# Optimization experiments

Hardware: AMD Instinct MI355X
Metric: run time of the kernel (lower is better)

## Reference

```python
import jax, jax.numpy as jnp
import numpy as np

N = 50000      # nodes
E = 800000     # edges (avg degree 16)
G = 8          # graphs in batch
D = 128        # in/hidden feats
C = 10         # classes


def setup_inputs() -> dict:
    key = jax.random.key(0)
    ks = jax.random.split(key, 9)
    x = jax.random.normal(ks[0], (N, D), dtype=jnp.float32)
    edge_index = jax.random.randint(ks[1], (2, E), 0, N)
    node2graph = jnp.sort(jax.random.randint(ks[2], (N,), 0, G))
    s = 1.0 / np.sqrt(D)
    W1 = jax.random.normal(ks[3], (D, D), dtype=jnp.float32) * s
    b1 = jnp.zeros((D,), jnp.float32)
    W2 = jax.random.normal(ks[4], (D, D), dtype=jnp.float32) * s
    b2 = jnp.zeros((D,), jnp.float32)
    Wl = jax.random.normal(ks[5], (D, C), dtype=jnp.float32) * s
    bl = jnp.zeros((C,), jnp.float32)
    return {"x": x, "edge_index": edge_index, "node2graph": node2graph,
            "W1": W1, "b1": b1, "W2": W2, "b2": b2, "Wl": Wl, "bl": bl}


def _graph_conv(h, src, dst, out_isqrt, in_isqrt, W, b):
    # DGL GraphConv, norm='both': D_in^{-1/2} A D_out^{-1/2} (h W) + b
    h = (h * out_isqrt[:, None]) @ W
    agg = jax.ops.segment_sum(h[src], dst, num_segments=N)  # SpMM gather/scatter
    return agg * in_isqrt[:, None] + b


def reference(x, edge_index, node2graph, W1, b1, W2, b2, Wl, bl):
    src, dst = edge_index[0], edge_index[1]
    ones_e = jnp.ones((E,), jnp.float32)
    out_deg = jnp.clip(jax.ops.segment_sum(ones_e, src, num_segments=N), 1.0)
    in_deg = jnp.clip(jax.ops.segment_sum(ones_e, dst, num_segments=N), 1.0)
    out_isqrt = jax.lax.rsqrt(out_deg)
    in_isqrt = jax.lax.rsqrt(in_deg)

    h = jax.nn.relu(_graph_conv(x, src, dst, out_isqrt, in_isqrt, W1, b1))
    h = jax.nn.relu(_graph_conv(h, src, dst, out_isqrt, in_isqrt, W2, b2))

    # AvgPooling: per-graph mean of node features
    sums = jax.ops.segment_sum(h, node2graph, num_segments=G)
    counts = jnp.clip(jax.ops.segment_sum(jnp.ones((N,), jnp.float32), node2graph, num_segments=G), 1.0)
    hg = sums / counts[:, None]

    logits = hg @ Wl + bl
    return jax.nn.softmax(logits, axis=1)
```

## Files before the change

kernel.cpp:

```cpp
#include <hip/hip_runtime.h>
#include <stdint.h>

#define FD 128
#define NG 8
#define NC 10
#define MAXB 1024
#define CHUNK 4096

typedef __attribute__((ext_vector_type(8))) short bf16x8;
typedef __attribute__((ext_vector_type(4))) float f32x4;
typedef __attribute__((ext_vector_type(2))) float f32x2;

__device__ __forceinline__ float bf2f(uint16_t u){
    union { uint32_t i; float f; } v; v.i = ((uint32_t)u) << 16; return v.f;
}
__device__ __forceinline__ uint16_t f2bf(float f){
    union { float f; uint32_t i; } v; v.f = f;
    uint32_t r = v.i + 0x7fff + ((v.i >> 16) & 1);
    return (uint16_t)(r >> 16);
}

#if __has_builtin(__builtin_amdgcn_cvt_pk_f32_fp8) && __has_builtin(__builtin_amdgcn_cvt_pk_fp8_f32)
__device__ __forceinline__ f32x2 fp8lo2f(uint32_t p){
    return __builtin_amdgcn_cvt_pk_f32_fp8((int)p, false);
}
__device__ __forceinline__ f32x2 fp8hi2f(uint32_t p){
    return __builtin_amdgcn_cvt_pk_f32_fp8((int)p, true);
}
__device__ __forceinline__ uint32_t pk4fp8(float a, float b, float c, float d){
    int u = 0;
    u = __builtin_amdgcn_cvt_pk_fp8_f32(a, b, u, false);
    u = __builtin_amdgcn_cvt_pk_fp8_f32(c, d, u, true);
    return (uint32_t)u;
}
#else
__device__ __forceinline__ float fp8tof(uint32_t b){
    union { uint32_t i; float f; } v;
    v.i = ((b & 0x7f) << 20) | ((b & 0x80) << 24);
    return v.f * 0x1p120f;
}
__device__ __forceinline__ f32x2 fp8lo2f(uint32_t p){
    return (f32x2){fp8tof(p & 0xff), fp8tof((p >> 8) & 0xff)};
}
__device__ __forceinline__ f32x2 fp8hi2f(uint32_t p){
    return (f32x2){fp8tof((p >> 16) & 0xff), fp8tof((p >> 24) & 0xff)};
}
__device__ __forceinline__ uint32_t f2fp8(float f){
    union { float f; uint32_t i; } v; v.f = f;
    uint32_t s = (v.i >> 24) & 0x80;
    float a = fabsf(f);
    if (a < 0x1p-10f) return s;
    if (a > 448.f) return s | 0x7e;
    v.f = a;
    uint32_t r = v.i + 0x7ffff + ((v.i >> 20) & 1);
    int e = (int)(r >> 23) - 127 + 7;
    uint32_t m = (r >> 20) & 7;
    if (e <= 0){
        uint32_t q = (uint32_t)(a * 512.f + 0.5f);
        return s | (q > 7 ? 8 : q);
    }
    if (e > 15) return s | 0x7e;
    return s | ((uint32_t)e << 3) | m;
}
__device__ __forceinline__ uint32_t pk4fp8(float a, float b, float c, float d){
    return (uint32_t)f2fp8(a) | ((uint32_t)f2fp8(b)<<8) |
           ((uint32_t)f2fp8(c)<<16) | ((uint32_t)f2fp8(d)<<24);
}
#endif

__global__ __launch_bounds__(256) void k_prep(const float* __restrict__ W1,
        const float* __restrict__ W2, uint16_t* Wf1, uint16_t* Wf2,
        const int* __restrict__ ei, int E, int B, int C, int shift,
        int* __restrict__ cnt, float* __restrict__ pool,
        unsigned long long* __restrict__ state, int* __restrict__ counters){
    int t = threadIdx.x;
    if (blockIdx.x < 128){
        int id = blockIdx.x*256 + t;
        int w = id >> 14;
        int r = id & 16383;
        int j = r & 7, frag = r >> 3;
        int lane = frag & 63, t2 = frag >> 6;
        int n = t2 & 7, kk = t2 >> 3;
        int k = kk*32 + (lane>>4)*8 + j;
        int col = n*16 + (lane&15);
        float v = (w ? W2 : W1)[k*128 + col];
        (w ? Wf2 : Wf1)[r] = f2bf(v);
        if (blockIdx.x == 0){
            for (int i = t; i < NG*FD; i += 256) pool[i] = 0.f;
            for (int i = t; i < 1024; i += 256) state[i] = 0ull;
            if (t < 8) counters[t] = 0;
        }
        return;
    }
    __shared__ int hd[MAXB], hs[MAXB];
    int c = blockIdx.x - 128;
    for (int i=t;i<B;i+=256){ hd[i]=0; hs[i]=0; }
    __syncthreads();
    int e0 = c*CHUNK, e1 = min(E, e0+CHUNK);
    for (int e = e0+t; e < e1; e += 256){
        int s = ei[e], d = ei[E+e];
        atomicAdd(&hd[d>>shift], 1);
        atomicAdd(&hs[s>>shift], 1);
    }
    __syncthreads();
    for (int i=t;i<B;i+=256){
        cnt[(size_t)i*C + c]     = hd[i];
        cnt[(size_t)(B+i)*C + c] = hs[i];
    }
}

#define SEPT 16
#define STILE 4096
__global__ __launch_bounds__(256) void k_scan(int* __restrict__ a, int M,
        unsigned long long* __restrict__ state, int* __restrict__ ticket){
    __shared__ int bid_s, exc_s;
    __shared__ int s[256];
    int t = threadIdx.x;
    if (t == 0) bid_s = atomicAdd(ticket, 1);
    __syncthreads();
    int bid = bid_s;
    int base = bid*STILE + t*SEPT;
    int v[SEPT]; int sum = 0;
    #pragma unroll
    for (int i=0;i<SEPT;i++){ int idx=base+i; int x=(idx<M)?a[idx]:0; v[i]=sum; sum+=x; }
    s[t]=sum; __syncthreads();
    for (int o=1;o<256;o<<=1){ int x=(t>=o)?s[t-o]:0; __syncthreads(); s[t]+=x; __syncthreads(); }
    int tot = s[255];
    int te = s[t]-sum;
    if (t == 0){
        unsigned long long pub = ((bid==0) ? (2ull<<62) : (1ull<<62)) | (unsigned long long)(unsigned)tot;
        __hip_atomic_store(&state[bid], pub, __ATOMIC_RELEASE, __HIP_MEMORY_SCOPE_AGENT);
        int exc = 0;
        if (bid > 0){
            int p = bid-1;
            while (true){
                unsigned long long st = __hip_atomic_load(&state[p], __ATOMIC_ACQUIRE, __HIP_MEMORY_SCOPE_AGENT);
                unsigned long long fl = st >> 62;
                if (fl == 2ull){ exc += (int)(unsigned)st; break; }
                if (fl == 1ull){ exc += (int)(unsigned)st; p--; }
            }
            __hip_atomic_store(&state[bid],
                (2ull<<62) | (unsigned long long)(unsigned)(exc + tot),
                __ATOMIC_RELEASE, __HIP_MEMORY_SCOPE_AGENT);
        }
        exc_s = exc;
    }
    __syncthreads();
    int exc = exc_s;
    #pragma unroll
    for (int i=0;i<SEPT;i++){ int idx=base+i; if (idx<M) a[idx]=exc+te+v[i]; }
}

__global__ __launch_bounds__(256) void k_scatter(const int* __restrict__ ei, int E,
        int B, int C, int shift, const int* __restrict__ scan,
        uint32_t* __restrict__ tempD, uint16_t* __restrict__ tempS){
    __shared__ int cd[MAXB], cs[MAXB];
    int t = threadIdx.x, c = blockIdx.x;
    for (int i=t;i<B;i+=256){
        cd[i] = scan[(size_t)i*C + c];
        cs[i] = scan[(size_t)(B+i)*C + c] - E;
    }
    __syncthreads();
    int e0 = c*CHUNK, e1 = min(E, e0+CHUNK);
    int lmask = (1<<shift) - 1;
    for (int e = e0+t; e < e1; e += 256){
        int s = ei[e], d = ei[E+e];
        int p = atomicAdd(&cd[d>>shift], 1);
        tempD[p] = ((uint32_t)(d & lmask) << 20) | (uint32_t)s;
        int q = atomicAdd(&cs[s>>shift], 1);
        tempS[q] = (uint16_t)s;
    }
}

__global__ __launch_bounds__(256) void k_build2(const uint32_t* __restrict__ tempD,
        const uint16_t* __restrict__ tempS, const int* __restrict__ scan,
        int B, int C, int shift, int E, int N,
        int* __restrict__ row_off, int* __restrict__ csr, int* __restrict__ deg_out){
    __shared__ int cnt[MAXB];
    __shared__ int offl[MAXB];
    int b = blockIdx.x, t = threadIdx.x;
    int range = 1<<shift, nb0 = b<<shift;
    int seg0 = scan[(size_t)b*C];
    int seg1 = (b+1<B) ? scan[(size_t)(b+1)*C] : E;
    for (int i=t;i<range;i+=256) cnt[i]=0;
    __syncthreads();
    for (int i=seg0+t; i<seg1; i+=256)
        atomicAdd(&cnt[tempD[i]>>20], 1);
    __syncthreads();
    if (t==0){ int run=0; for (int i=0;i<range;i++){ offl[i]=run; run+=cnt[i]; } }
    __syncthreads();
    for (int i=t;i<range;i+=256){
        int node = nb0+i;
        if (node < N) row_off[node] = seg0 + offl[i];
    }
    if (b==B-1 && t==0) row_off[N] = E;
    for (int i=t;i<range;i+=256) cnt[i] = offl[i];
    __syncthreads();
    for (int i=seg0+t; i<seg1; i+=256){
        uint32_t v = tempD[i];
        int p = atomicAdd(&cnt[v>>20], 1);
        csr[seg0 + p] = (int)(v & 0xFFFFFu);
    }
    __syncthreads();
    int sg0 = scan[(size_t)(B+b)*C] - E;
    int sg1 = ((b+1<B) ? scan[(size_t)(B+b+1)*C] : 2*E) - E;
    for (int i=t;i<range;i+=256) cnt[i]=0;
    __syncthreads();
    for (int i=sg0+t; i<sg1; i+=256)
        atomicAdd(&cnt[(int)tempS[i] - nb0], 1);
    __syncthreads();
    for (int i=t;i<range;i+=256){
        int node = nb0+i;
        if (node < N) deg_out[node] = cnt[i];
    }
}

__global__ __launch_bounds__(256) void k_gemm(const void* __restrict__ A,
        const uint16_t* __restrict__ Wf, const int* __restrict__ deg_out,
        uint8_t* __restrict__ out8, int nrows, int amode){
    int t = threadIdx.x;
    int wave = t>>6, lane = t&63, quad = lane>>4, low = lane&15;

    int rowA  = blockIdx.x*64 + wave*16 + low;
    int rowAc = min(rowA, nrows-1);

    bf16x8 ah[4];
    if (amode){
        const uint16_t* arow = (const uint16_t*)A + (size_t)rowAc*FD;
        #pragma unroll
        for (int kk=0;kk<4;kk++)
            ah[kk] = *(const bf16x8*)(arow + kk*32 + quad*8);
    } else {
        const float* arow = (const float*)A + (size_t)rowAc*FD;
        #pragma unroll
        for (int kk=0;kk<4;kk++){
            f32x4 f0 = *(const f32x4*)(arow + kk*32 + quad*8);
            f32x4 f1 = *(const f32x4*)(arow + kk*32 + quad*8 + 4);
            #pragma unroll
            for (int j=0;j<4;j++) ah[kk][j]   = (short)f2bf(f0[j]);
            #pragma unroll
            for (int j=0;j<4;j++) ah[kk][j+4] = (short)f2bf(f1[j]);
        }
    }

    f32x4 acc[8];
    #pragma unroll
    for (int n=0;n<8;n++) acc[n] = (f32x4){0.f,0.f,0.f,0.f};

    #pragma unroll
    for (int kk=0;kk<4;kk++){
        #pragma unroll
        for (int n=0;n<8;n++){
            bf16x8 bh = *(const bf16x8*)(Wf + ((size_t)((kk*8+n)*64 + lane))*8);
            acc[n] = __builtin_amdgcn_mfma_f32_16x16x32_bf16(bh, ah[kk], acc[n], 0, 0, 0);
        }
    }

    if (rowA < nrows){
        float sc = rsqrtf((float)max(deg_out[rowA], 1));
        uint8_t* orow = out8 + (size_t)rowA*FD;
        #pragma unroll
        for (int n=0;n<8;n++){
            uint32_t pk = pk4fp8(acc[n][0]*sc, acc[n][1]*sc, acc[n][2]*sc, acc[n][3]*sc);
            *(uint32_t*)(orow + n*16 + quad*4) = pk;
        }
    }
}

__device__ __forceinline__ void spmm_row(const uint2* __restrict__ tp,
        const int* __restrict__ csr_src, int e0, int e1, int l, int qb,
        f32x2& a01, f32x2& a23, f32x2& a45, f32x2& a67){
    for (int base = e0; base < e1; base += 16){
        int my = 0;
        if (base + l < e1) my = csr_src[base + l];
        int cnt = min(16, e1 - base);
        for (int j0 = 0; j0 < cnt; j0 += 8){
            int ss[8];
            #pragma unroll
            for (int k=0;k<8;k++)
                ss[k] = __shfl(my, qb + min(j0 + k, cnt-1));
            uint2 p[8];
            #pragma unroll
            for (int k=0;k<8;k++)
                p[k] = tp[(size_t)ss[k]*16 + l];
            #pragma unroll
            for (int k=0;k<8;k++){
                if (j0 + k < cnt){
                    a01 += fp8lo2f(p[k].x); a23 += fp8hi2f(p[k].x);
                    a45 += fp8lo2f(p[k].y); a67 += fp8hi2f(p[k].y);
                }
            }
        }
    }
}

__global__ __launch_bounds__(256) void k_spmm_gemm(const uint8_t* __restrict__ tmp8,
        const int* __restrict__ row_off, const int* __restrict__ csr_src,
        const float* __restrict__ bias, const uint16_t* __restrict__ Wf,
        const int* __restrict__ deg_out, uint8_t* __restrict__ out8, int N){
    __shared__ __align__(16) uint16_t hsrow[64][136];
    int tid = threadIdx.x;
    int l = tid & 15, qid = tid >> 4, qb = (tid & 63) & 48;
    const uint2* tp = (const uint2*)tmp8;
    f32x4 bv0 = *(const f32x4*)(bias + l*8);
    f32x4 bv1 = *(const f32x4*)(bias + l*8 + 4);
    #pragma unroll
    for (int i = 0; i < 4; i++){
        int rowL = qid*4 + i;
        int node = blockIdx.x*64 + rowL;
        int e0 = 0, e1 = 0;
        if (node < N){ e0 = row_off[node]; e1 = row_off[node+1]; }
        f32x2 a01={0.f,0.f}, a23={0.f,0.f}, a45={0.f,0.f}, a67={0.f,0.f};
        spmm_row(tp, csr_src, e0, e1, l, qb, a01, a23, a45, a67);
        float isq = rsqrtf((float)max(e1 - e0, 1));
        float r0 = fmaxf(a01.x*isq + bv0[0], 0.f);
        float r1 = fmaxf(a01.y*isq + bv0[1], 0.f);
        float r2 = fmaxf(a23.x*isq + bv0[2], 0.f);
        float r3 = fmaxf(a23.y*isq + bv0[3], 0.f);
        float r4 = fmaxf(a45.x*isq + bv1[0], 0.f);
        float r5 = fmaxf(a45.y*isq + bv1[1], 0.f);
        float r6 = fmaxf(a67.x*isq + bv1[2], 0.f);
        float r7 = fmaxf(a67.y*isq + bv1[3], 0.f);
        uint4 o;
        o.x = (uint32_t)f2bf(r0) | ((uint32_t)f2bf(r1) << 16);
        o.y = (uint32_t)f2bf(r2) | ((uint32_t)f2bf(r3) << 16);
        o.z = (uint32_t)f2bf(r4) | ((uint32_t)f2bf(r5) << 16);
        o.w = (uint32_t)f2bf(r6) | ((uint32_t)f2bf(r7) << 16);
        if (node >= N) o = (uint4){0u,0u,0u,0u};
        *(uint4*)(&hsrow[rowL][l*8]) = o;
    }
    __syncthreads();
    int wave = tid>>6, lane = tid&63, quad = lane>>4, low = lane&15;
    int rowL = wave*16 + low;
    int rowA = blockIdx.x*64 + rowL;
    bf16x8 ah[4];
    #pragma unroll
    for (int kk=0;kk<4;kk++)
        ah[kk] = *(const bf16x8*)(&hsrow[rowL][kk*32 + quad*8]);
    f32x4 acc[8];
    #pragma unroll
    for (int n=0;n<8;n++) acc[n] = (f32x4){0.f,0.f,0.f,0.f};
    #pragma unroll
    for (int kk=0;kk<4;kk++){
        #pragma unroll
        for (int n=0;n<8;n++){
            bf16x8 bh = *(const bf16x8*)(Wf + ((size_t)((kk*8+n)*64 + lane))*8);
            acc[n] = __builtin_amdgcn_mfma_f32_16x16x32_bf16(bh, ah[kk], acc[n], 0, 0, 0);
        }
    }
    if (rowA < N){
        float sc = rsqrtf((float)max(deg_out[rowA], 1));
        uint8_t* orow = out8 + (size_t)rowA*FD;
        #pragma unroll
        for (int n=0;n<8;n++){
            uint32_t pk = pk4fp8(acc[n][0]*sc, acc[n][1]*sc, acc[n][2]*sc, acc[n][3]*sc);
            *(uint32_t*)(orow + n*16 + quad*4) = pk;
        }
    }
}

__global__ __launch_bounds__(256) void k_spmm_pool(const uint8_t* __restrict__ tmp8,
        const int* __restrict__ row_off, const int* __restrict__ csr_src,
        const float* __restrict__ bias, const int* __restrict__ n2g,
        float* __restrict__ pool, int N){
    __shared__ float sacc[NG*FD];
    int tid = threadIdx.x;
    for (int i = tid; i < NG*FD; i += 256) sacc[i] = 0.f;
    __syncthreads();
    int l = tid & 15, qid = tid >> 4, qb = (tid & 63) & 48;
    const uint2* tp = (const uint2*)tmp8;
    f32x4 bv0 = *(const f32x4*)(bias + l*8);
    f32x4 bv1 = *(const f32x4*)(bias + l*8 + 4);
    int rg = -1;
    float racc[8];
    #pragma unroll
    for (int j=0;j<8;j++) racc[j] = 0.f;
    #pragma unroll
    for (int i = 0; i < 4; i++){
        int node = blockIdx.x*64 + qid*4 + i;
        if (node < N){
            int e0 = row_off[node], e1 = row_off[node+1];
            f32x2 a01={0.f,0.f}, a23={0.f,0.f}, a45={0.f,0.f}, a67={0.f,0.f};
            spmm_row(tp, csr_src, e0, e1, l, qb, a01, a23, a45, a67);
            float isq = rsqrtf((float)max(e1 - e0, 1));
            float r[8];
            r[0] = fmaxf(a01.x*isq + bv0[0], 0.f);
            r[1] = fmaxf(a01.y*isq + bv0[1], 0.f);
            r[2] = fmaxf(a23.x*isq + bv0[2], 0.f);
            r[3] = fmaxf(a23.y*isq + bv0[3], 0.f);
            r[4] = fmaxf(a45.x*isq + bv1[0], 0.f);
            r[5] = fmaxf(a45.y*isq + bv1[1], 0.f);
            r[6] = fmaxf(a67.x*isq + bv1[2], 0.f);
            r[7] = fmaxf(a67.y*isq + bv1[3], 0.f);
            int g = n2g[node];
            if (g != rg){
                if (rg >= 0){
                    #pragma unroll
                    for (int j=0;j<8;j++) atomicAdd(&sacc[rg*FD + l*8 + j], racc[j]);
                }
                rg = g;
                #pragma unroll
                for (int j=0;j<8;j++) racc[j] = 0.f;
            }
            #pragma unroll
            for (int j=0;j<8;j++) racc[j] += r[j];
        }
    }
    if (rg >= 0){
        #pragma unroll
        for (int j=0;j<8;j++) atomicAdd(&sacc[rg*FD + l*8 + j], racc[j]);
    }
    __syncthreads();
    for (int i = tid; i < NG*FD; i += 256){
        float v = sacc[i];
        if (v != 0.f) atomicAdd(&pool[i], v);
    }
}

__global__ __launch_bounds__(128) void k_final(const float* __restrict__ pool,
        const int* __restrict__ n2g, int N, const float* __restrict__ Wl,
        const float* __restrict__ bl, float* __restrict__ out){
    __shared__ int ub[NG+1];
    __shared__ float logits[NG][NC];
    int t = threadIdx.x;
    if (t <= NG){
        int lo = 0, hi = N;
        while (lo < hi){ int mid = (lo+hi)>>1; if (n2g[mid] < t) lo = mid+1; else hi = mid; }
        ub[t] = lo;
    }
    __syncthreads();
    if (t < NG*NC){
        int g = t/NC, c = t%NC;
        float cnt = (float)max(ub[g+1]-ub[g], 1);
        float inv = 1.f/cnt;
        float acc = bl[c];
        for (int d=0; d<FD; d++)
            acc += pool[g*FD+d]*inv * Wl[d*NC+c];
        logits[g][c] = acc;
    }
    __syncthreads();
    if (t < NG*NC){
        int g = t/NC, c = t%NC;
        float m = -1e30f;
        for (int i=0;i<NC;i++) m = fmaxf(m, logits[g][i]);
        float ssum = 0.f;
        for (int i=0;i<NC;i++) ssum += expf(logits[g][i]-m);
        out[t] = expf(logits[g][c]-m)/ssum;
    }
}

extern "C" void kernel_launch(void* const* d_in, const int* in_sizes, int n_in,
                              void* d_out, int out_size, void* d_ws, size_t ws_size,
                              hipStream_t stream) {
    const float* x   = (const float*)d_in[0];
    const int*   ei  = (const int*)d_in[1];
    const int*   n2g = (const int*)d_in[2];
    const float* W1  = (const float*)d_in[3];
    const float* b1  = (const float*)d_in[4];
    const float* W2  = (const float*)d_in[5];
    const float* b2  = (const float*)d_in[6];
    const float* Wl  = (const float*)d_in[7];
    const float* bl  = (const float*)d_in[8];
    float* outp = (float*)d_out;

    int N = in_sizes[2];
    int E = in_sizes[1] / 2;

    int shift = 6;
    while ((((N + (1<<shift) - 1) >> shift) > MAXB) && shift < 10) shift++;
    int B = (N + (1<<shift) - 1) >> shift;
    int C = (E + CHUNK - 1) / CHUNK;
    int M = 2*B*C;
    int nscan = (M + STILE - 1) / STILE;

    char* w = (char*)d_ws;
    size_t off = 0;
    auto alloc = [&](size_t bytes)->char*{ char* p = w + off; off += (bytes + 255) & ~(size_t)255; return p; };
    float*    pool    = (float*)alloc((size_t)NG*FD*4);
    unsigned long long* state = (unsigned long long*)alloc(1024*8);
    int*      counters= (int*)alloc(8*4);
    int*      deg_out = (int*)alloc((size_t)N*4);
    int*      row_off = (int*)alloc((size_t)(N+1)*4);
    int*      csr     = (int*)alloc((size_t)E*4);
    uint16_t* Wf1     = (uint16_t*)alloc(16384*2);
    uint16_t* Wf2     = (uint16_t*)alloc(16384*2);
    uint8_t*  tmp8    = (uint8_t*)alloc((size_t)N*FD);
    uint8_t*  tmp8b   = (uint8_t*)alloc((size_t)N*FD);
    int*      cnt     = (int*)alloc((size_t)M*4);
    (void)ws_size;
    uint32_t* tempD = (uint32_t*)tmp8;
    uint16_t* tempS = (uint16_t*)(tmp8 + (size_t)E*4);

    k_prep   <<<128 + C, 256, 0, stream>>>(W1, W2, Wf1, Wf2, ei, E, B, C, shift,
                                           cnt, pool, state, counters);
    k_scan   <<<nscan, 256, 0, stream>>>(cnt, M, state, &counters[0]);
    k_scatter<<<C, 256, 0, stream>>>(ei, E, B, C, shift, cnt, tempD, tempS);
    k_build2 <<<B, 256, 0, stream>>>(tempD, tempS, cnt, B, C, shift, E, N, row_off, csr, deg_out);

    int gb = (N + 63)/64;
    k_gemm      <<<gb, 256, 0, stream>>>(x, Wf1, deg_out, tmp8, N, 0);
    k_spmm_gemm <<<gb, 256, 0, stream>>>(tmp8,  row_off, csr, b1, Wf2, deg_out, tmp8b, N);
    k_spmm_pool <<<gb, 256, 0, stream>>>(tmp8b, row_off, csr, b2, n2g, pool, N);
    k_final     <<<1,  128, 0, stream>>>(pool, n2g, N, Wl, bl, outp);
}
```

Before: 223.3 us.

## Replace scan-based CSR build with fixed-capacity bucket slots via global atomics

Drops the per-chunk histogram plus decoupled-lookback scan and instead reserves space in fixed-capacity per-bucket regions (CAP entries per bucket) using global atomicAdd on bucket_fill. Out-degree is now counted with global atomics directly in the scatter kernel rather than via a separate source-sorted pass, and row ends come from a new deg_in array. This removes one kernel launch, the scan pass and the tempS traffic. In exchange it uses more workspace and silently drops edges if a bucket overflows CAP.

```diff
diff --git a/kernel.cpp b/kernel.cpp
--- a/kernel.cpp
+++ b/kernel.cpp
@@ -70,12 +70,11 @@
 
 __global__ __launch_bounds__(256) void k_prep(const float* __restrict__ W1,
         const float* __restrict__ W2, uint16_t* Wf1, uint16_t* Wf2,
-        const int* __restrict__ ei, int E, int B, int C, int shift,
-        int* __restrict__ cnt, float* __restrict__ pool,
-        unsigned long long* __restrict__ state, int* __restrict__ counters){
+        int N, int B, int* __restrict__ deg_out, int* __restrict__ bucket_fill,
+        float* __restrict__ pool){
     int t = threadIdx.x;
-    if (blockIdx.x < 128){
-        int id = blockIdx.x*256 + t;
+    int id = blockIdx.x*256 + t;
+    {
         int w = id >> 14;
         int r = id & 16383;
         int j = r & 7, frag = r >> 3;
@@ -85,133 +84,100 @@
         int col = n*16 + (lane&15);
         float v = (w ? W2 : W1)[k*128 + col];
         (w ? Wf2 : Wf1)[r] = f2bf(v);
-        if (blockIdx.x == 0){
-            for (int i = t; i < NG*FD; i += 256) pool[i] = 0.f;
-            for (int i = t; i < 1024; i += 256) state[i] = 0ull;
-            if (t < 8) counters[t] = 0;
-        }
-        return;
-    }
-    __shared__ int hd[MAXB], hs[MAXB];
-    int c = blockIdx.x - 128;
-    for (int i=t;i<B;i+=256){ hd[i]=0; hs[i]=0; }
+    }
+    for (int i = id; i < N; i += 32768) deg_out[i] = 0;
+    for (int i = id; i < B; i += 32768) bucket_fill[i] = 0;
+    if (id < NG*FD) pool[id] = 0.f;
+}
+
+__global__ __launch_bounds__(256) void k_scatter(const int* __restrict__ ei,
+        int E, int B, int shift, int CAP,
+        int* __restrict__ bucket_fill, int* __restrict__ deg_out,
+        uint32_t* __restrict__ tempD){
+    __shared__ int hc[MAXB];
+    __shared__ int hb_[MAXB];
+    int t = threadIdx.x, c = blockIdx.x;
+    for (int i=t;i<B;i+=256) hc[i]=0;
     __syncthreads();
     int e0 = c*CHUNK, e1 = min(E, e0+CHUNK);
-    for (int e = e0+t; e < e1; e += 256){
-        int s = ei[e], d = ei[E+e];
-        atomicAdd(&hd[d>>shift], 1);
-        atomicAdd(&hs[s>>shift], 1);
+    int ss[16], dd[16];
+    #pragma unroll
+    for (int k=0;k<16;k++){
+        int e = e0 + t + k*256;
+        bool ok = e < e1;
+        int s = ok ? ei[e]   : 0;
+        int d = ok ? ei[E+e] : 0;
+        ss[k] = s; dd[k] = ok ? d : -1;
+        if (ok){
+            atomicAdd(&hc[d>>shift], 1);
+            atomicAdd(&deg_out[s], 1);
+        }
     }
     __syncthreads();
     for (int i=t;i<B;i+=256){
-        cnt[(size_t)i*C + c]     = hd[i];
-        cnt[(size_t)(B+i)*C + c] = hs[i];
-    }
-}
-
-#define SEPT 16
-#define STILE 4096
-__global__ __launch_bounds__(256) void k_scan(int* __restrict__ a, int M,
-        unsigned long long* __restrict__ state, int* __restrict__ ticket){
-    __shared__ int bid_s, exc_s;
-    __shared__ int s[256];
-    int t = threadIdx.x;
-    if (t == 0) bid_s = atomicAdd(ticket, 1);
-    __syncthreads();
-    int bid = bid_s;
-    int base = bid*STILE + t*SEPT;
-    int v[SEPT]; int sum = 0;
-    #pragma unroll
-    for (int i=0;i<SEPT;i++){ int idx=base+i; int x=(idx<M)?a[idx]:0; v[i]=sum; sum+=x; }
-    s[t]=sum; __syncthreads();
-    for (int o=1;o<256;o<<=1){ int x=(t>=o)?s[t-o]:0; __syncthreads(); s[t]+=x; __syncthreads(); }
-    int tot = s[255];
-    int te = s[t]-sum;
-    if (t == 0){
-        unsigned long long pub = ((bid==0) ? (2ull<<62) : (1ull<<62)) | (unsigned long long)(unsigned)tot;
-        __hip_atomic_store(&state[bid], pub, __ATOMIC_RELEASE, __HIP_MEMORY_SCOPE_AGENT);
-        int exc = 0;
-        if (bid > 0){
-            int p = bid-1;
-            while (true){
-                unsigned long long st = __hip_atomic_load(&state[p], __ATOMIC_ACQUIRE, __HIP_MEMORY_SCOPE_AGENT);
-                unsigned long long fl = st >> 62;
-                if (fl == 2ull){ exc += (int)(unsigned)st; break; }
-                if (fl == 1ull){ exc += (int)(unsigned)st; p--; }
-            }
-            __hip_atomic_store(&state[bid],
-                (2ull<<62) | (unsigned long long)(unsigned)(exc + tot),
-                __ATOMIC_RELEASE, __HIP_MEMORY_SCOPE_AGENT);
-        }
-        exc_s = exc;
-    }
-    __syncthreads();
-    int exc = exc_s;
-    #pragma unroll
-    for (int i=0;i<SEPT;i++){ int idx=base+i; if (idx<M) a[idx]=exc+te+v[i]; }
-}
-
-__global__ __launch_bounds__(256) void k_scatter(const int* __restrict__ ei, int E,
-        int B, int C, int shift, const int* __restrict__ scan,
-        uint32_t* __restrict__ tempD, uint16_t* __restrict__ tempS){
-    __shared__ int cd[MAXB], cs[MAXB];
-    int t = threadIdx.x, c = blockIdx.x;
-    for (int i=t;i<B;i+=256){
-        cd[i] = scan[(size_t)i*C + c];
-        cs[i] = scan[(size_t)(B+i)*C + c] - E;
-    }
-    __syncthreads();
-    int e0 = c*CHUNK, e1 = min(E, e0+CHUNK);
+        int cn = hc[i];
+        hb_[i] = cn ? atomicAdd(&bucket_fill[i], cn) : 0;
+    }
+    __syncthreads();
+    for (int i=t;i<B;i+=256) hc[i]=0;
+    __syncthreads();
     int lmask = (1<<shift) - 1;
-    for (int e = e0+t; e < e1; e += 256){
-        int s = ei[e], d = ei[E+e];
-        int p = atomicAdd(&cd[d>>shift], 1);
-        tempD[p] = ((uint32_t)(d & lmask) << 20) | (uint32_t)s;
-        int q = atomicAdd(&cs[s>>shift], 1);
-        tempS[q] = (uint16_t)s;
-    }
-}
-
-__global__ __launch_bounds__(256) void k_build2(const uint32_t* __restrict__ tempD,
-        const uint16_t* __restrict__ tempS, const int* __restrict__ scan,
-        int B, int C, int shift, int E, int N,
-        int* __restrict__ row_off, int* __restrict__ csr, int* __restrict__ deg_out){
-    __shared__ int cnt[MAXB];
-    __shared__ int offl[MAXB];
+    #pragma unroll
+    for (int k=0;k<16;k++){
+        int d = dd[k];
+        if (d >= 0){
+            int b = d >> shift;
+            int p = hb_[b] + atomicAdd(&hc[b], 1);
+            if (p < CAP)
+                tempD[(size_t)b*CAP + p] = ((uint32_t)(d & lmask) << 20) | (uint32_t)ss[k];
+        }
+    }
+}
+
+__global__ __launch_bounds__(256) void k_build(const uint32_t* __restrict__ tempD,
+        const int* __restrict__ bucket_fill, int B, int shift, int N, int CAP,
+        int* __restrict__ row_off, int* __restrict__ deg_in, int* __restrict__ csr){
+    __shared__ int cnt_[MAXB];
+    __shared__ int off_[MAXB];
     int b = blockIdx.x, t = threadIdx.x;
     int range = 1<<shift, nb0 = b<<shift;
-    int seg0 = scan[(size_t)b*C];
-    int seg1 = (b+1<B) ? scan[(size_t)(b+1)*C] : E;
-    for (int i=t;i<range;i+=256) cnt[i]=0;
-    __syncthreads();
-    for (int i=seg0+t; i<seg1; i+=256)
-        atomicAdd(&cnt[tempD[i]>>20], 1);
-    __syncthreads();
-    if (t==0){ int run=0; for (int i=0;i<range;i++){ offl[i]=run; run+=cnt[i]; } }
-    __syncthreads();
+    int fill = min(bucket_fill[b], CAP);
+    const uint32_t* seg = tempD + (size_t)b*CAP;
+    for (int i=t;i<range;i+=256) cnt_[i]=0;
+    __syncthreads();
+    for (int i=t;i<fill;i+=256)
+        atomicAdd(&cnt_[seg[i]>>20], 1);
+    __syncthreads();
+    if (range == 64){
+        if (t < 64){
+            int v = cnt_[t];
+            int inc = v;
+            #pragma unroll
+            for (int o=1;o<64;o<<=1){
+                int u = __shfl_up(inc, o);
+                if (t >= o) inc += u;
+            }
+            off_[t] = inc - v;
+        }
+    } else if (t == 0){
+        int run = 0;
+        for (int i=0;i<range;i++){ off_[i]=run; run+=cnt_[i]; }
+    }
+    __syncthreads();
+    int base = b*CAP;
     for (int i=t;i<range;i+=256){
-        int node = nb0+i;
-        if (node < N) row_off[node] = seg0 + offl[i];
-    }
-    if (b==B-1 && t==0) row_off[N] = E;
-    for (int i=t;i<range;i+=256) cnt[i] = offl[i];
-    __syncthreads();
-    for (int i=seg0+t; i<seg1; i+=256){
-        uint32_t v = tempD[i];
-        int p = atomicAdd(&cnt[v>>20], 1);
-        csr[seg0 + p] = (int)(v & 0xFFFFFu);
-    }
-    __syncthreads();
-    int sg0 = scan[(size_t)(B+b)*C] - E;
-    int sg1 = ((b+1<B) ? scan[(size_t)(B+b+1)*C] : 2*E) - E;
-    for (int i=t;i<range;i+=256) cnt[i]=0;
-    __syncthreads();
-    for (int i=sg0+t; i<sg1; i+=256)
-        atomicAdd(&cnt[(int)tempS[i] - nb0], 1);
-    __syncthreads();
-    for (int i=t;i<range;i+=256){
-        int node = nb0+i;
-        if (node < N) deg_out[node] = cnt[i];
+        int node = nb0 + i;
+        if (node < N){
+            row_off[node] = base + off_[i];
+            deg_in[node]  = cnt_[i];
+        }
+    }
+    __syncthreads();
+    int* csrb = csr + (size_t)base;
+    for (int i=t;i<fill;i+=256){
+        uint32_t v = seg[i];
+        int p = atomicAdd(&off_[v>>20], 1);
+        csrb[p] = (int)(v & 0xFFFFFu);
     }
 }
 
@@ -295,7 +261,8 @@
 }
 
 __global__ __launch_bounds__(256) void k_spmm_gemm(const uint8_t* __restrict__ tmp8,
-        const int* __restrict__ row_off, const int* __restrict__ csr_src,
+        const int* __restrict__ row_off, const int* __restrict__ deg_in,
+        const int* __restrict__ csr_src,
         const float* __restrict__ bias, const uint16_t* __restrict__ Wf,
         const int* __restrict__ deg_out, uint8_t* __restrict__ out8, int N){
     __shared__ __align__(16) uint16_t hsrow[64][136];
@@ -309,7 +276,7 @@
         int rowL = qid*4 + i;
         int node = blockIdx.x*64 + rowL;
         int e0 = 0, e1 = 0;
-        if (node < N){ e0 = row_off[node]; e1 = row_off[node+1]; }
+        if (node < N){ e0 = row_off[node]; e1 = e0 + deg_in[node]; }
         f32x2 a01={0.f,0.f}, a23={0.f,0.f}, a45={0.f,0.f}, a67={0.f,0.f};
         spmm_row(tp, csr_src, e0, e1, l, qb, a01, a23, a45, a67);
         float isq = rsqrtf((float)max(e1 - e0, 1));
@@ -360,7 +327,8 @@
 }
 
 __global__ __launch_bounds__(256) void k_spmm_pool(const uint8_t* __restrict__ tmp8,
-        const int* __restrict__ row_off, const int* __restrict__ csr_src,
+        const int* __restrict__ row_off, const int* __restrict__ deg_in,
+        const int* __restrict__ csr_src,
         const float* __restrict__ bias, const int* __restrict__ n2g,
         float* __restrict__ pool, int N){
     __shared__ float sacc[NG*FD];
@@ -379,7 +347,7 @@
     for (int i = 0; i < 4; i++){
         int node = blockIdx.x*64 + qid*4 + i;
         if (node < N){
-            int e0 = row_off[node], e1 = row_off[node+1];
+            int e0 = row_off[node], e1 = e0 + deg_in[node];
             f32x2 a01={0.f,0.f}, a23={0.f,0.f}, a45={0.f,0.f}, a67={0.f,0.f};
             spmm_row(tp, csr_src, e0, e1, l, qb, a01, a23, a45, a67);
             float isq = rsqrtf((float)max(e1 - e0, 1));
@@ -470,36 +438,33 @@
     while ((((N + (1<<shift) - 1) >> shift) > MAXB) && shift < 10) shift++;
     int B = (N + (1<<shift) - 1) >> shift;
     int C = (E + CHUNK - 1) / CHUNK;
-    int M = 2*B*C;
-    int nscan = (M + STILE - 1) / STILE;
+    int meanFill = (int)(((long long)E << shift) / (N > 0 ? N : 1)) + 1;
+    int CAP = 4096;
+    while (CAP < 4*meanFill) CAP <<= 1;
 
     char* w = (char*)d_ws;
     size_t off = 0;
     auto alloc = [&](size_t bytes)->char*{ char* p = w + off; off += (bytes + 255) & ~(size_t)255; return p; };
-    float*    pool    = (float*)alloc((size_t)NG*FD*4);
-    unsigned long long* state = (unsigned long long*)alloc(1024*8);
-    int*      counters= (int*)alloc(8*4);
-    int*      deg_out = (int*)alloc((size_t)N*4);
-    int*      row_off = (int*)alloc((size_t)(N+1)*4);
-    int*      csr     = (int*)alloc((size_t)E*4);
-    uint16_t* Wf1     = (uint16_t*)alloc(16384*2);
-    uint16_t* Wf2     = (uint16_t*)alloc(16384*2);
-    uint8_t*  tmp8    = (uint8_t*)alloc((size_t)N*FD);
-    uint8_t*  tmp8b   = (uint8_t*)alloc((size_t)N*FD);
-    int*      cnt     = (int*)alloc((size_t)M*4);
+    float*    pool        = (float*)alloc((size_t)NG*FD*4);
+    int*      deg_out     = (int*)alloc((size_t)N*4);
+    int*      deg_in      = (int*)alloc((size_t)N*4);
+    int*      row_off     = (int*)alloc((size_t)N*4);
+    int*      bucket_fill = (int*)alloc((size_t)MAXB*4);
+    uint16_t* Wf1         = (uint16_t*)alloc(16384*2);
+    uint16_t* Wf2         = (uint16_t*)alloc(16384*2);
+    uint32_t* tempD       = (uint32_t*)alloc((size_t)B*CAP*4);
+    int*      csr         = (int*)alloc((size_t)B*CAP*4);
+    uint8_t*  tmp8        = (uint8_t*)alloc((size_t)N*FD);
+    uint8_t*  tmp8b       = (uint8_t*)alloc((size_t)N*FD);
     (void)ws_size;
-    uint32_t* tempD = (uint32_t*)tmp8;
-    uint16_t* tempS = (uint16_t*)(tmp8 + (size_t)E*4);
-
-    k_prep   <<<128 + C, 256, 0, stream>>>(W1, W2, Wf1, Wf2, ei, E, B, C, shift,
-                                           cnt, pool, state, counters);
-    k_scan   <<<nscan, 256, 0, stream>>>(cnt, M, state, &counters[0]);
-    k_scatter<<<C, 256, 0, stream>>>(ei, E, B, C, shift, cnt, tempD, tempS);
-    k_build2 <<<B, 256, 0, stream>>>(tempD, tempS, cnt, B, C, shift, E, N, row_off, csr, deg_out);
+
+    k_prep   <<<128, 256, 0, stream>>>(W1, W2, Wf1, Wf2, N, B, deg_out, bucket_fill, pool);
+    k_scatter<<<C,   256, 0, stream>>>(ei, E, B, shift, CAP, bucket_fill, deg_out, tempD);
+    k_build  <<<B,   256, 0, stream>>>(tempD, bucket_fill, B, shift, N, CAP, row_off, deg_in, csr);
 
     int gb = (N + 63)/64;
     k_gemm      <<<gb, 256, 0, stream>>>(x, Wf1, deg_out, tmp8, N, 0);
-    k_spmm_gemm <<<gb, 256, 0, stream>>>(tmp8,  row_off, csr, b1, Wf2, deg_out, tmp8b, N);
-    k_spmm_pool <<<gb, 256, 0, stream>>>(tmp8b, row_off, csr, b2, n2g, pool, N);
+    k_spmm_gemm <<<gb, 256, 0, stream>>>(tmp8,  row_off, deg_in, csr, b1, Wf2, deg_out, tmp8b, N);
+    k_spmm_pool <<<gb, 256, 0, stream>>>(tmp8b, row_off, deg_in, csr, b2, n2g, pool, N);
     k_final     <<<1,  128, 0, stream>>>(pool, n2g, N, Wl, bl, outp);
 }
```

Measured after the change: 218.6 us. 2.1% less time.
